# Performance work log

Hardware: AMD Instinct MI355X
Metric: run time of the kernel (lower is better)

## Reference

```python
import jax, jax.numpy as jnp
import numpy as np

HEADS = 12

def setup_inputs() -> dict:
    key = jax.random.key(0)
    k1, k2, k3 = jax.random.split(key, 3)
    b, n, d = 8, 1024, 768
    x = jax.random.normal(k1, (b, n, d), dtype=jnp.float32)
    # xavier_uniform-like init for linear weights
    lim_qkv = float(np.sqrt(6.0 / (d + 3 * d)))
    W_qkv = jax.random.uniform(k2, (3 * d, d), dtype=jnp.float32, minval=-lim_qkv, maxval=lim_qkv)
    b_qkv = jnp.zeros((3 * d,), dtype=jnp.float32)
    lim_o = float(np.sqrt(6.0 / (d + d)))
    W_out = jax.random.uniform(k3, (d, d), dtype=jnp.float32, minval=-lim_o, maxval=lim_o)
    b_out = jnp.zeros((d,), dtype=jnp.float32)
    return {"x": x, "W_qkv": W_qkv, "b_qkv": b_qkv, "W_out": W_out, "b_out": b_out}

def reference(x, W_qkv, b_qkv, W_out, b_out):
    b, n, d = x.shape
    h = HEADS
    hd = d // h
    scale = d ** (-0.5)  # NOTE: original scales by dim**-0.5, not head_dim**-0.5
    qkv = x @ W_qkv.T + b_qkv                      # [b, n, 3d]
    q, k, v = jnp.split(qkv, 3, axis=-1)           # each [b, n, d]
    def to_heads(t):
        return t.reshape(b, n, h, hd).transpose(0, 2, 1, 3)  # [b, h, n, hd]
    q, k, v = to_heads(q), to_heads(k), to_heads(v)
    dots = jnp.einsum('bhid,bhjd->bhij', q, k) * scale       # [b, h, n, n]
    attn = jax.nn.softmax(dots, axis=-1)
    out = jnp.einsum('bhij,bhjd->bhid', attn, v)             # [b, h, n, hd]
    out = out.transpose(0, 2, 1, 3).reshape(b, n, d)
    return out @ W_out.T + b_out
```

## Files before the change

kernel.cpp:

```cpp
#include <hip/hip_runtime.h>
#include <stdint.h>

typedef __bf16 bf16x8 __attribute__((ext_vector_type(8)));
typedef float  f32x4  __attribute__((ext_vector_type(4)));
typedef unsigned short u16;

#define AS1 __attribute__((address_space(1)))
#define AS3 __attribute__((address_space(3)))
#define G2L(gp, lp) __builtin_amdgcn_global_load_lds( \
    (const AS1 unsigned int*)(uintptr_t)(gp), \
    (AS3 unsigned int*)(uintptr_t)(lp), 16, 0, 0)

static __device__ __forceinline__ u16 f32_to_bf16(float f) {
    unsigned u = __float_as_uint(f);
    u += 0x7fffu + ((u >> 16) & 1u);
    return (u16)(u >> 16);
}

static __device__ __forceinline__ unsigned pack_bf16(float lo, float hi) {
    return (unsigned)f32_to_bf16(lo) | ((unsigned)f32_to_bf16(hi) << 16);
}

static __device__ __forceinline__ float fast_exp2(float x) {
    return __builtin_amdgcn_exp2f(x);
}

static __device__ __forceinline__ f32x4 mfma16(bf16x8 a, bf16x8 b, f32x4 c) {
    return __builtin_amdgcn_mfma_f32_16x16x32_bf16(a, b, c, 0, 0, 0);
}

__global__ void cvt3_k(const float* __restrict__ a, const float* __restrict__ b,
                       const float* __restrict__ c, u16* __restrict__ out) {
    const int i = blockIdx.x * blockDim.x + threadIdx.x;
    const float* src; int off;
    if (i < 1572864)      { src = a; off = 0; }
    else if (i < 2015232) { src = b; off = 1572864; }
    else                  { src = c; off = 2015232; }
    const float4 v = reinterpret_cast<const float4*>(src)[i - off];
    reinterpret_cast<uint2*>(out)[i] = make_uint2(pack_bf16(v.x, v.y), pack_bf16(v.z, v.w));
}

template<int OUTF32>
__global__ __launch_bounds__(256, 2) void gemm_bt_k(const u16* __restrict__ A, const u16* __restrict__ B,
                                                    const float* __restrict__ bias, void* __restrict__ Cp,
                                                    int M, int N, int K, int nbx, int qcols, float qsc) {
    __shared__ __align__(16) u16 As[2][2][128 * 32];
    __shared__ __align__(16) u16 Bs[2][2][128 * 32];
    const int id = blockIdx.x;
    const int cpx = gridDim.x >> 3;
    const int swz = (id & 7) * cpx + (id >> 3);
    const int bx = swz % nbx, by = swz / nbx;
    const int t = threadIdx.x, w = t >> 6, l = t & 63, lr = l & 15, lg = l >> 4;
    const int wr = w >> 1, wc = w & 1;
    const long rowBase = (long)by * 128;
    const long colBase = (long)bx * 128;

    const f32x4 z = {0.f, 0.f, 0.f, 0.f};
    f32x4 acc[4][4];
    #pragma unroll
    for (int m = 0; m < 4; ++m)
        #pragma unroll
        for (int n = 0; n < 4; ++n) acc[m][n] = z;

    const int kSteps = K >> 6;

    #define STAGE_U(kt, h) do {                                                     \
        const int k0_ = ((kt) << 6) + (h) * 32;                                     \
        const int bi_ = (kt) & 1;                                                   \
        _Pragma("unroll")                                                           \
        for (int i_ = 0; i_ < 2; ++i_) {                                            \
            const int c_ = i_ * 256 + t, row_ = c_ >> 2, ch_ = c_ & 3;              \
            const int sch_ = ch_ ^ ((row_ >> 1) & 3);                               \
            G2L(A + (rowBase + row_) * K + k0_ + sch_ * 8, &As[bi_][h][(i_ * 256 + w * 64) * 8]); \
            G2L(B + (colBase + row_) * K + k0_ + sch_ * 8, &Bs[bi_][h][(i_ * 256 + w * 64) * 8]); \
        }                                                                           \
    } while (0)

    #define COMPUTE_H(h) do {                                                       \
        bf16x8 af[4], bfr[4];                                                       \
        _Pragma("unroll")                                                           \
        for (int m = 0; m < 4; ++m) {                                               \
            const int row = wr * 64 + m * 16 + lr;                                  \
            af[m] = *reinterpret_cast<const bf16x8*>(&As[cur][h][row * 32 + ((lg ^ ((row >> 1) & 3)) << 3)]); \
        }                                                                           \
        _Pragma("unroll")                                                           \
        for (int n = 0; n < 4; ++n) {                                               \
            const int row = wc * 64 + n * 16 + lr;                                  \
            bfr[n] = *reinterpret_cast<const bf16x8*>(&Bs[cur][h][row * 32 + ((lg ^ ((row >> 1) & 3)) << 3)]); \
        }                                                                           \
        _Pragma("unroll")                                                           \
        for (int m = 0; m < 4; ++m)                                                 \
            _Pragma("unroll")                                                       \
            for (int n = 0; n < 4; ++n) acc[m][n] = mfma16(af[m], bfr[n], acc[m][n]); \
    } while (0)

    STAGE_U(0, 0); STAGE_U(0, 1); STAGE_U(1, 0);
    for (int kt = 0; kt < kSteps; ++kt) {
        const int cur = kt & 1;
        if (kt + 1 < kSteps) asm volatile("s_waitcnt vmcnt(8)" ::: "memory");
        else                 asm volatile("s_waitcnt vmcnt(4)" ::: "memory");
        __builtin_amdgcn_sched_barrier(0);
        __builtin_amdgcn_s_barrier();
        __builtin_amdgcn_sched_barrier(0);
        if (kt + 1 < kSteps) STAGE_U(kt + 1, 1);
        COMPUTE_H(0);
        if (kt + 1 < kSteps) asm volatile("s_waitcnt vmcnt(8)" ::: "memory");
        else                 asm volatile("s_waitcnt vmcnt(0)" ::: "memory");
        __builtin_amdgcn_sched_barrier(0);
        __builtin_amdgcn_s_barrier();
        __builtin_amdgcn_sched_barrier(0);
        if (kt + 2 < kSteps) STAGE_U(kt + 2, 0);
        COMPUTE_H(1);
    }
    #undef STAGE_U
    #undef COMPUTE_H

    #pragma unroll
    for (int n = 0; n < 4; ++n) {
        const long gc = colBase + wc * 64 + n * 16 + lr;
        const float bv = bias[gc];
        const float csc = (gc < qcols) ? qsc : 1.0f;
        #pragma unroll
        for (int m = 0; m < 4; ++m) {
            const long gr = rowBase + wr * 64 + m * 16 + lg * 4;
            #pragma unroll
            for (int r = 0; r < 4; ++r) {
                const float v = (acc[m][n][r] + bv) * csc;
                if (OUTF32) reinterpret_cast<float*>(Cp)[(gr + r) * N + gc] = v;
                else        reinterpret_cast<u16*>(Cp)[(gr + r) * N + gc] = f32_to_bf16(v);
            }
        }
    }
}

__global__ __launch_bounds__(256) void transpose_v_k(const u16* __restrict__ qkv, u16* __restrict__ vt) {
    const int bh = blockIdx.y, b = bh / 12, h = bh % 12;
    const int nt = blockIdx.x;
    __shared__ __align__(16) u16 Ts[64][72];
    const int t = threadIdx.x;
    const int rr = t >> 2;
    #pragma unroll
    for (int i = 0; i < 2; ++i) {
        const int ch = (t & 3) + i * 4;
        const u16* src = qkv + (long)(b * 1024 + nt * 64 + rr) * 2304 + 1536 + h * 64 + ch * 8;
        *reinterpret_cast<uint4*>(&Ts[rr][ch * 8]) = *reinterpret_cast<const uint4*>(src);
    }
    __syncthreads();
    #pragma unroll
    for (int i = 0; i < 2; ++i) {
        const int ch = (t & 3) + i * 4;
        u16 vals[8];
        #pragma unroll
        for (int j = 0; j < 8; ++j)
            vals[j] = Ts[(ch >> 2) * 32 + (j >> 2) * 16 + (ch & 3) * 4 + (j & 3)][rr];
        u16* dst = vt + (long)(bh * 64 + rr) * 1024 + nt * 64 + ch * 8;
        *reinterpret_cast<uint4*>(dst) = *reinterpret_cast<const uint4*>(vals);
    }
}

__global__ __launch_bounds__(256, 3) void attn_k(const u16* __restrict__ qkv, const u16* __restrict__ vt,
                                                 u16* __restrict__ outp) {
    const int id = blockIdx.x;
    const int bh = id % 96, qt = id / 96;
    const int b = bh / 12, h = bh % 12;
    const int t = threadIdx.x, w = t >> 6, l = t & 63, lr = l & 15, lg = l >> 4;
    __shared__ __align__(16) u16 Ks[2][64 * 64];
    __shared__ __align__(16) u16 Vts[2][64 * 64];

    const u16* kb = qkv + 768 + h * 64;
    const u16* vb = vt + (long)bh * 64 * 1024;

    #pragma unroll
    for (int i = 0; i < 2; ++i) {
        const int c = (i * 4 + w) * 64 + l;
        const int row = c >> 3, sch = (c & 7) ^ (row & 7);
        G2L(kb + (long)(b * 1024 + row) * 2304 + sch * 8, &Ks[0][(i * 4 + w) * 512]);
        G2L(vb + (long)row * 1024 + sch * 8, &Vts[0][(i * 4 + w) * 512]);
    }
    const u16* qb = qkv + (long)(b * 1024 + qt * 128 + w * 32) * 2304 + h * 64;
    bf16x8 aq[2][2];
    #pragma unroll
    for (int qf = 0; qf < 2; ++qf)
        #pragma unroll
        for (int kk = 0; kk < 2; ++kk)
            aq[qf][kk] = *reinterpret_cast<const bf16x8*>(qb + (long)(qf * 16 + lr) * 2304 + (kk * 4 + lg) * 8);

    const f32x4 z = {0.f, 0.f, 0.f, 0.f};
    f32x4 o[2][4];
    f32x4 dacc[2];
    #pragma unroll
    for (int qf = 0; qf < 2; ++qf) {
        #pragma unroll
        for (int n = 0; n < 4; ++n) o[qf][n] = z;
        dacc[qf] = z;
    }
    const unsigned one2 = 0x3F803F80u;
    uint4 onesu = make_uint4(one2, one2, one2, one2);
    const bf16x8 ones = *reinterpret_cast<const bf16x8*>(&onesu);

    #pragma unroll 2
    for (int kt = 0; kt < 16; ++kt) {
        const int cur = kt & 1;
        asm volatile("s_waitcnt vmcnt(0)" ::: "memory");
        __builtin_amdgcn_sched_barrier(0);
        __builtin_amdgcn_s_barrier();
        __builtin_amdgcn_sched_barrier(0);
        if (kt < 15) {
            const int ktn = kt + 1;
            #pragma unroll
            for (int i = 0; i < 2; ++i) {
                const int c = (i * 4 + w) * 64 + l;
                const int row = c >> 3, sch = (c & 7) ^ (row & 7);
                G2L(kb + (long)(b * 1024 + ktn * 64 + row) * 2304 + sch * 8, &Ks[cur ^ 1][(i * 4 + w) * 512]);
                G2L(vb + (long)row * 1024 + ktn * 64 + sch * 8, &Vts[cur ^ 1][(i * 4 + w) * 512]);
            }
        }
        __builtin_amdgcn_sched_barrier(0);
        f32x4 s[4][2];
        #pragma unroll
        for (int kc = 0; kc < 4; ++kc)
            #pragma unroll
            for (int qf = 0; qf < 2; ++qf) s[kc][qf] = z;
        #pragma unroll
        for (int kk = 0; kk < 2; ++kk) {
            #pragma unroll
            for (int kc = 0; kc < 4; ++kc) {
                const int row = kc * 16 + lr;
                bf16x8 bk = *reinterpret_cast<const bf16x8*>(&Ks[cur][row * 64 + (((kk * 4 + lg) ^ (lr & 7)) << 3)]);
                s[kc][0] = mfma16(bk, aq[0][kk], s[kc][0]);
                s[kc][1] = mfma16(bk, aq[1][kk], s[kc][1]);
            }
        }
        #pragma unroll
        for (int qf = 0; qf < 2; ++qf) {
            float pv[4][4];
            #pragma unroll
            for (int kc = 0; kc < 4; ++kc)
                #pragma unroll
                for (int r = 0; r < 4; ++r)
                    pv[kc][r] = fast_exp2(s[kc][qf][r]);
            uint4 u0, u1;
            u0.x = pack_bf16(pv[0][0], pv[0][1]); u0.y = pack_bf16(pv[0][2], pv[0][3]);
            u0.z = pack_bf16(pv[1][0], pv[1][1]); u0.w = pack_bf16(pv[1][2], pv[1][3]);
            u1.x = pack_bf16(pv[2][0], pv[2][1]); u1.y = pack_bf16(pv[2][2], pv[2][3]);
            u1.z = pack_bf16(pv[3][0], pv[3][1]); u1.w = pack_bf16(pv[3][2], pv[3][3]);
            bf16x8 pa0 = *reinterpret_cast<bf16x8*>(&u0);
            bf16x8 pa1 = *reinterpret_cast<bf16x8*>(&u1);
            dacc[qf] = mfma16(pa0, ones, dacc[qf]);
            dacc[qf] = mfma16(pa1, ones, dacc[qf]);
            #pragma unroll
            for (int kk = 0; kk < 2; ++kk) {
                const bf16x8 pa = kk ? pa1 : pa0;
                const int swzk = ((kk * 4 + lg) ^ (lr & 7)) << 3;
                #pragma unroll
                for (int n = 0; n < 4; ++n) {
                    const int row = n * 16 + lr;
                    bf16x8 vbf = *reinterpret_cast<const bf16x8*>(&Vts[cur][row * 64 + swzk]);
                    o[qf][n] = mfma16(pa, vbf, o[qf][n]);
                }
            }
        }
    }
    #pragma unroll
    for (int qf = 0; qf < 2; ++qf) {
        const int qrow = qt * 128 + w * 32 + qf * 16 + lg * 4;
        #pragma unroll
        for (int r = 0; r < 4; ++r) {
            const float inv = 1.0f / dacc[qf][r];
            #pragma unroll
            for (int n = 0; n < 4; ++n) {
                outp[(long)(b * 1024 + qrow + r) * 768 + h * 64 + n * 16 + lr] =
                    f32_to_bf16(o[qf][n][r] * inv);
            }
        }
    }
}

extern "C" void kernel_launch(void* const* d_in, const int* in_sizes, int n_in,
                              void* d_out, int out_size, void* d_ws, size_t ws_size,
                              hipStream_t stream) {
    (void)in_sizes; (void)n_in; (void)out_size; (void)ws_size;
    const float* x    = (const float*)d_in[0];
    const float* Wqkv = (const float*)d_in[1];
    const float* bqkv = (const float*)d_in[2];
    const float* Wout = (const float*)d_in[3];
    const float* bout = (const float*)d_in[4];

    u16* xb   = (u16*)d_ws;
    u16* Wqb  = xb  + 6291456;
    u16* Wob  = Wqb + 1769472;
    u16* qkv  = Wob + 589824;
    u16* vtb  = qkv + 18874368;
    u16* attn = vtb + 6291456;

    const float sc2 = 0.052058773f;

    cvt3_k<<<8448, 256, 0, stream>>>(x, Wqkv, Wout, xb);

    gemm_bt_k<0><<<1152, 256, 0, stream>>>(xb, Wqb, bqkv, qkv, 8192, 2304, 768, 18, 768, sc2);
    transpose_v_k<<<dim3(16, 96), 256, 0, stream>>>(qkv, vtb);
    attn_k<<<768, 256, 0, stream>>>(qkv, vtb, attn);
    gemm_bt_k<1><<<384, 256, 0, stream>>>(attn, Wob, bout, d_out, 8192, 768, 768, 6, 0, 1.0f);
}
```

Measured before the change: 111.6 us.

## Load A fragments directly from global into registers, stage only B in LDS

The GEMM now skips LDS for the A operand: each wave reads its A rows straight from global memory into registers, double-buffered across k-steps, and only B goes through LDS with a 64-wide XOR swizzle. The goal is to halve LDS traffic and footprint and drop the split-half pipeline. The cost is that the two waves sharing the same A rows now both fetch them from global, more VGPRs are spent on register double-buffering, and each step waits on vmcnt(0), so less load latency is hidden. The loop also assumes an even number of k-steps.

```diff
diff --git a/kernel.cpp b/kernel.cpp
--- a/kernel.cpp
+++ b/kernel.cpp
@@ -44,8 +44,7 @@
 __global__ __launch_bounds__(256, 2) void gemm_bt_k(const u16* __restrict__ A, const u16* __restrict__ B,
                                                     const float* __restrict__ bias, void* __restrict__ Cp,
                                                     int M, int N, int K, int nbx, int qcols, float qsc) {
-    __shared__ __align__(16) u16 As[2][2][128 * 32];
-    __shared__ __align__(16) u16 Bs[2][2][128 * 32];
+    __shared__ __align__(16) u16 Bs[2][128 * 64];
     const int id = blockIdx.x;
     const int cpx = gridDim.x >> 3;
     const int swz = (id & 7) * cpx + (id >> 3);
@@ -63,57 +62,67 @@
         for (int n = 0; n < 4; ++n) acc[m][n] = z;
 
     const int kSteps = K >> 6;
-
-    #define STAGE_U(kt, h) do {                                                     \
-        const int k0_ = ((kt) << 6) + (h) * 32;                                     \
-        const int bi_ = (kt) & 1;                                                   \
+    const u16* aBase = A + (rowBase + wr * 64 + lr) * (long)K;
+
+    #define STAGE_B(kt, bi) do {                                                    \
+        const int k0_ = (kt) << 6;                                                  \
         _Pragma("unroll")                                                           \
-        for (int i_ = 0; i_ < 2; ++i_) {                                            \
-            const int c_ = i_ * 256 + t, row_ = c_ >> 2, ch_ = c_ & 3;              \
-            const int sch_ = ch_ ^ ((row_ >> 1) & 3);                               \
-            G2L(A + (rowBase + row_) * K + k0_ + sch_ * 8, &As[bi_][h][(i_ * 256 + w * 64) * 8]); \
-            G2L(B + (colBase + row_) * K + k0_ + sch_ * 8, &Bs[bi_][h][(i_ * 256 + w * 64) * 8]); \
+        for (int i_ = 0; i_ < 4; ++i_) {                                            \
+            const int c_ = i_ * 256 + t, row_ = c_ >> 3, ch_ = c_ & 7;              \
+            const int sch_ = ch_ ^ (row_ & 7);                                      \
+            G2L(B + (colBase + row_) * K + k0_ + sch_ * 8, &Bs[bi][(i_ * 256 + w * 64) * 8]); \
         }                                                                           \
     } while (0)
 
-    #define COMPUTE_H(h) do {                                                       \
-        bf16x8 af[4], bfr[4];                                                       \
+    #define LOAD_A(DST, kt) do {                                                    \
+        const int k0_ = (kt) << 6;                                                  \
         _Pragma("unroll")                                                           \
-        for (int m = 0; m < 4; ++m) {                                               \
-            const int row = wr * 64 + m * 16 + lr;                                  \
-            af[m] = *reinterpret_cast<const bf16x8*>(&As[cur][h][row * 32 + ((lg ^ ((row >> 1) & 3)) << 3)]); \
+        for (int kk_ = 0; kk_ < 2; ++kk_)                                           \
+            _Pragma("unroll")                                                       \
+            for (int m_ = 0; m_ < 4; ++m_)                                          \
+                DST[kk_ * 4 + m_] = *reinterpret_cast<const bf16x8*>(               \
+                    aBase + (long)m_ * 16 * K + k0_ + (kk_ * 4 + lg) * 8);          \
+    } while (0)
+
+    #define BODY(kt, CUR, NXT) do {                                                 \
+        const int cur_ = (kt) & 1;                                                  \
+        asm volatile("s_waitcnt vmcnt(0)" ::: "memory");                            \
+        __builtin_amdgcn_sched_barrier(0);                                          \
+        __builtin_amdgcn_s_barrier();                                               \
+        __builtin_amdgcn_sched_barrier(0);                                          \
+        if ((kt) + 1 < kSteps) {                                                    \
+            STAGE_B((kt) + 1, cur_ ^ 1);                                            \
+            LOAD_A(NXT, (kt) + 1);                                                  \
         }                                                                           \
+        __builtin_amdgcn_sched_barrier(0);                                          \
         _Pragma("unroll")                                                           \
-        for (int n = 0; n < 4; ++n) {                                               \
-            const int row = wc * 64 + n * 16 + lr;                                  \
-            bfr[n] = *reinterpret_cast<const bf16x8*>(&Bs[cur][h][row * 32 + ((lg ^ ((row >> 1) & 3)) << 3)]); \
+        for (int kk_ = 0; kk_ < 2; ++kk_) {                                         \
+            bf16x8 bfr_[4];                                                         \
+            _Pragma("unroll")                                                       \
+            for (int n_ = 0; n_ < 4; ++n_) {                                        \
+                const int row_ = wc * 64 + n_ * 16 + lr;                            \
+                bfr_[n_] = *reinterpret_cast<const bf16x8*>(                        \
+                    &Bs[cur_][row_ * 64 + (((kk_ * 4 + lg) ^ (lr & 7)) << 3)]);     \
+            }                                                                       \
+            _Pragma("unroll")                                                       \
+            for (int m_ = 0; m_ < 4; ++m_)                                          \
+                _Pragma("unroll")                                                   \
+                for (int n_ = 0; n_ < 4; ++n_)                                      \
+                    acc[m_][n_] = mfma16(CUR[kk_ * 4 + m_], bfr_[n_], acc[m_][n_]); \
         }                                                                           \
-        _Pragma("unroll")                                                           \
-        for (int m = 0; m < 4; ++m)                                                 \
-            _Pragma("unroll")                                                       \
-            for (int n = 0; n < 4; ++n) acc[m][n] = mfma16(af[m], bfr[n], acc[m][n]); \
     } while (0)
 
-    STAGE_U(0, 0); STAGE_U(0, 1); STAGE_U(1, 0);
-    for (int kt = 0; kt < kSteps; ++kt) {
-        const int cur = kt & 1;
-        if (kt + 1 < kSteps) asm volatile("s_waitcnt vmcnt(8)" ::: "memory");
-        else                 asm volatile("s_waitcnt vmcnt(4)" ::: "memory");
-        __builtin_amdgcn_sched_barrier(0);
-        __builtin_amdgcn_s_barrier();
-        __builtin_amdgcn_sched_barrier(0);
-        if (kt + 1 < kSteps) STAGE_U(kt + 1, 1);
-        COMPUTE_H(0);
-        if (kt + 1 < kSteps) asm volatile("s_waitcnt vmcnt(8)" ::: "memory");
-        else                 asm volatile("s_waitcnt vmcnt(0)" ::: "memory");
-        __builtin_amdgcn_sched_barrier(0);
-        __builtin_amdgcn_s_barrier();
-        __builtin_amdgcn_sched_barrier(0);
-        if (kt + 2 < kSteps) STAGE_U(kt + 2, 0);
-        COMPUTE_H(1);
-    }
-    #undef STAGE_U
-    #undef COMPUTE_H
+    bf16x8 afA[8], afB[8];
+    STAGE_B(0, 0);
+    LOAD_A(afA, 0);
+    const int kPairs = kSteps >> 1;
+    for (int kp = 0; kp < kPairs; ++kp) {
+        BODY(2 * kp, afA, afB);
+        BODY(2 * kp + 1, afB, afA);
+    }
+    #undef STAGE_B
+    #undef LOAD_A
+    #undef BODY
 
     #pragma unroll
     for (int n = 0; n < 4; ++n) {
```

After: 154.4 us. 1.38x slower.
